# Performance work log

Measured on AMD Instinct MI355X. Metric: run time of the kernel, lower is better.

Reference implementation:

```python
import jax, jax.numpy as jnp
import numpy as np

DIM = 512
N = 64
DIV = 8
H = DIM // DIV  # 64
BATCH = 8
L_SEQ = 2048


def _kernel_dplr(Lam, P, B, C, step, L):
    # Lam: (N,) complex, P: (N,1), B: (N,H), C: (H,N), step: scalar
    omega = jnp.exp(-2j * jnp.pi * (jnp.arange(L) / L))        # (L,)
    g = (2.0 / step) * (1.0 - omega) / (1.0 + omega)           # (L,) generating-fn nodes
    c = 2.0 / (1.0 + omega)                                    # (L,)
    r = 1.0 / (g[:, None] - Lam[None, :])                      # (L,N) Cauchy resolvent
    Cc = jnp.conj(C)                                           # (H,N)
    p = P[:, 0]                                                # (N,)
    pc = jnp.conj(p)
    # vectorized Cauchy dot-products (torch version loops over L)
    k00 = jnp.einsum('in,nj,ln->lij', Cc, B, r)                # (L,H,H)
    k01 = jnp.einsum('in,n,ln->li', Cc, p, r)                  # (L,H)
    k10 = jnp.einsum('n,nj,ln->lj', pc, B, r)                  # (L,H)
    k11 = jnp.einsum('n,n,ln->l', pc, p, r)                    # (L,)
    # woodbury correction: inv(1 + k11) is a 1x1 batched inverse -> elementwise
    at_roots = c[:, None, None] * (
        k00 - k01[:, :, None] * (1.0 / (1.0 + k11))[:, None, None] * k10[:, None, :]
    )                                                          # (L,H,H)
    return jnp.fft.ifft(at_roots, n=L, axis=0).real            # (L,H,H)


def _fft_conv(u, K):
    # u: (b,L,H) real, K: (L,H,H) real. Linear conv via length-2L FFT.
    L = K.shape[0]
    ud = jnp.fft.rfft(u, n=2 * L, axis=1)                      # (b,Lf,H)
    Kd = jnp.fft.rfft(K, n=2 * L, axis=0)                      # (Lf,H,H)
    yf = jnp.einsum('lij,blj->bli', Kd, ud)                    # (b,Lf,H)
    return jnp.fft.irfft(yf, n=2 * L, axis=1)[:, :L]           # (b,L,H)


def reference(u, Lambda_re, Lambda_im, P_re, P_im, B_re, B_im, C_re, C_im, step):
    # straight-through clamp of Lambda_re (torch does an in-place no_grad clamp)
    Lambda_re = Lambda_re + jax.lax.stop_gradient(
        jnp.minimum(Lambda_re, -1e-4) - Lambda_re)
    Lam = Lambda_re + 1j * Lambda_im                           # (N,div)
    P = P_re + 1j * P_im                                       # (N,1,div)
    Bm = B_re + 1j * B_im                                      # (N,H,div)
    Cm = C_re + 1j * C_im                                      # (H,N,div)
    b, L, d = u.shape
    u4 = u.reshape(b, L, d // DIV, DIV)                        # (b,L,H,div)
    s = jnp.exp(step)[0]
    K = jax.vmap(_kernel_dplr, in_axes=(-1, -1, -1, -1, None, None),
                 out_axes=-1)(Lam, P, Bm, Cm, s, L)            # (L,H,H,div)
    y = jax.vmap(_fft_conv, in_axes=(-1, -1), out_axes=-1)(u4, K)  # (b,L,H,div)
    return y.reshape(b, L, d)


def setup_inputs() -> dict:
    key = jax.random.key(0)
    ks = jax.random.split(key, 10)
    sc = 0.5 ** 0.5
    u = jax.random.normal(ks[0], (BATCH, L_SEQ, DIM), dtype=jnp.float32)
    Lambda_re = -(jax.random.uniform(ks[1], (N, DIV), dtype=jnp.float32) * 0.5 + 0.1)
    Lambda_im = jax.random.normal(ks[2], (N, DIV), dtype=jnp.float32)
    P_re = jax.random.normal(ks[3], (N, 1, DIV), dtype=jnp.float32) * sc
    P_im = jax.random.normal(ks[4], (N, 1, DIV), dtype=jnp.float32) * sc
    B_re = jax.random.normal(ks[5], (N, H, DIV), dtype=jnp.float32) * sc
    B_im = jax.random.normal(ks[6], (N, H, DIV), dtype=jnp.float32) * sc
    C_re = jax.random.normal(ks[7], (H, N, DIV), dtype=jnp.float32) * sc
    C_im = jax.random.normal(ks[8], (H, N, DIV), dtype=jnp.float32) * sc
    step = jax.random.uniform(ks[9], (1,), dtype=jnp.float32,
                              minval=float(np.log(0.001)), maxval=float(np.log(0.1)))
    return {"u": u, "Lambda_re": Lambda_re, "Lambda_im": Lambda_im,
            "P_re": P_re, "P_im": P_im, "B_re": B_re, "B_im": B_im,
            "C_re": C_re, "C_im": C_im, "step": step}
```

## Files before the change

kernel.cpp:

```cpp
#include <hip/hip_runtime.h>
#include <hip/hip_bf16.h>
#include <math.h>

#define LSEQ 2048
#define NM   64
#define HD   64
#define NDIV 8
#define NB   8
#define NF   2049
#define ATROWS 4224

#define SL(E) ((E) + ((E) >> 3))
#define FFT_BUF 2304

typedef __attribute__((ext_vector_type(8))) short bf16x8;
typedef __attribute__((ext_vector_type(4))) float f32x4;

__device__ __forceinline__ unsigned pack_c(float2 v) {
  __hip_bfloat162 h = __float22bfloat162_rn(v);
  return *reinterpret_cast<unsigned*>(&h);
}
__device__ __forceinline__ float2 unpack_c(unsigned u) {
  __hip_bfloat162 h = *reinterpret_cast<__hip_bfloat162*>(&u);
  return __bfloat1622float2(h);
}
__device__ __forceinline__ unsigned short f2bf(float v) {
  __hip_bfloat16 h = __float2bfloat16(v);
  return *reinterpret_cast<unsigned short*>(&h);
}

struct cplxd { double x, y; };
__device__ __forceinline__ cplxd cmuld(cplxd a, cplxd b) {
  return {a.x*b.x - a.y*b.y, a.x*b.y + a.y*b.x};
}
__device__ __forceinline__ cplxd cdivd(cplxd a, cplxd b) {
  double inv = 1.0 / (b.x*b.x + b.y*b.y);
  return {(a.x*b.x + a.y*b.y)*inv, (a.y*b.x - a.x*b.y)*inv};
}

template<int SIGN, int M>
__device__ __forceinline__ void r4_stage(const float2* __restrict__ src,
                                         float2* __restrict__ dst) {
  constexpr int L = 2048 / (4 * M);
  __syncthreads();
  #pragma unroll
  for (int t = 0; t < 2; t++) {
    int idx = (int)threadIdx.x + t * 256;
    int q = idx / M;
    int p = idx & (M - 1);
    float2 a0 = src[SL(idx)];
    float2 a1 = src[SL(idx + 512)];
    float2 a2 = src[SL(idx + 1024)];
    float2 a3 = src[SL(idx + 1536)];
    float2 b1, b2, b3;
    if constexpr (M > 1) {
      float s, c;
      __sincosf(-3.14159265358979324f * (float)(p * L) * (1.0f/1024.0f), &s, &c);
      float2 W1 = make_float2(c, (SIGN > 0) ? -s : s);
      float2 W2 = make_float2(W1.x*W1.x - W1.y*W1.y, 2.f*W1.x*W1.y);
      float2 W3 = make_float2(W2.x*W1.x - W2.y*W1.y, W2.x*W1.y + W2.y*W1.x);
      b1 = make_float2(a1.x*W1.x - a1.y*W1.y, a1.x*W1.y + a1.y*W1.x);
      b2 = make_float2(a2.x*W2.x - a2.y*W2.y, a2.x*W2.y + a2.y*W2.x);
      b3 = make_float2(a3.x*W3.x - a3.y*W3.y, a3.x*W3.y + a3.y*W3.x);
    } else { b1 = a1; b2 = a2; b3 = a3; }
    float2 e0 = make_float2(a0.x + b2.x, a0.y + b2.y);
    float2 e1 = make_float2(b1.x + b3.x, b1.y + b3.y);
    float2 d0 = make_float2(a0.x - b2.x, a0.y - b2.y);
    float2 d1 = make_float2(b1.x - b3.x, b1.y - b3.y);
    float2 o1, o3;
    if (SIGN < 0) { o1 = make_float2(d0.x + d1.y, d0.y - d1.x);
                    o3 = make_float2(d0.x - d1.y, d0.y + d1.x); }
    else          { o1 = make_float2(d0.x - d1.y, d0.y + d1.x);
                    o3 = make_float2(d0.x + d1.y, d0.y - d1.x); }
    int ob = q * 4 * M + p;
    dst[SL(ob)]         = make_float2(e0.x + e1.x, e0.y + e1.y);
    dst[SL(ob + M)]     = o1;
    dst[SL(ob + 2*M)]   = make_float2(e0.x - e1.x, e0.y - e1.y);
    dst[SL(ob + 3*M)]   = o3;
  }
}

template<int SIGN>
__device__ __forceinline__ void r4_mid(float2* a, float2* b) {
  r4_stage<SIGN,   4>(a, b);
  r4_stage<SIGN,  16>(b, a);
  r4_stage<SIGN,  64>(a, b);
  r4_stage<SIGN, 256>(b, a);
}

template<int SIGN>
__device__ __forceinline__ void r2f_ldst(const float2* __restrict__ src,
                                         float2* __restrict__ dst) {
  __syncthreads();
  #pragma unroll
  for (int t = 0; t < 4; t++) {
    int p = (int)threadIdx.x + t * 256;
    float2 a = src[SL(p)], b = src[SL(p + 1024)];
    float s, c;
    __sincosf(-6.28318530717958647f * (float)p * (1.0f/2048.0f), &s, &c);
    float wy = (SIGN > 0) ? -s : s;
    float2 wb = make_float2(b.x*c - b.y*wy, b.x*wy + b.y*c);
    dst[SL(p)]        = make_float2(a.x + wb.x, a.y + wb.y);
    dst[SL(p + 1024)] = make_float2(a.x - wb.x, a.y - wb.y);
  }
}

__device__ __forceinline__ void r4g_bf16_inv(const unsigned* __restrict__ row,
                                             float2* __restrict__ dst) {
  #pragma unroll
  for (int t = 0; t < 2; t++) {
    int idx = (int)threadIdx.x + t * 256;
    float2 a0 = unpack_c(row[idx]);
    float2 a1 = unpack_c(row[idx + 512]);
    float2 a2 = unpack_c(row[idx + 1024]);
    float2 a3 = unpack_c(row[idx + 1536]);
    float2 e0 = make_float2(a0.x + a2.x, a0.y + a2.y);
    float2 e1 = make_float2(a1.x + a3.x, a1.y + a3.y);
    float2 d0 = make_float2(a0.x - a2.x, a0.y - a2.y);
    float2 d1 = make_float2(a1.x - a3.x, a1.y - a3.y);
    float2 o1 = make_float2(d0.x - d1.y, d0.y + d1.x);
    float2 o3 = make_float2(d0.x + d1.y, d0.y - d1.x);
    int ob = idx * 4;
    dst[SL(ob)]   = make_float2(e0.x + e1.x, e0.y + e1.y);
    dst[SL(ob+1)] = o1;
    dst[SL(ob+2)] = make_float2(e0.x - e1.x, e0.y - e1.y);
    dst[SL(ob+3)] = o3;
  }
}

__device__ __forceinline__ void r4g_f32pad_fwd(const float2* __restrict__ g,
                                               float2* __restrict__ dst) {
  #pragma unroll
  for (int t = 0; t < 2; t++) {
    int idx = (int)threadIdx.x + t * 256;
    float2 a0 = g[idx];
    float2 a1 = g[idx + 512];
    int ob = idx * 4;
    dst[SL(ob)]   = make_float2(a0.x + a1.x, a0.y + a1.y);
    dst[SL(ob+1)] = make_float2(a0.x + a1.y, a0.y - a1.x);
    dst[SL(ob+2)] = make_float2(a0.x - a1.x, a0.y - a1.y);
    dst[SL(ob+3)] = make_float2(a0.x - a1.y, a0.y + a1.x);
  }
}

__device__ __forceinline__ void r4_modfused(const float2* __restrict__ pre,
                                            float2* __restrict__ dst) {
  __syncthreads();
  const float sc = 1.0f/2048.0f;
  const float R = 0.70710678118654752f;
  #pragma unroll
  for (int t = 0; t < 2; t++) {
    int idx = (int)threadIdx.x + t * 256;
    float a0x = pre[SL(idx)].x;
    float a1x = pre[SL(idx + 512)].x;
    float2 bA = pre[SL(idx + 1024)];
    float2 bB = pre[SL(idx + 1536)];
    float sA, cA, sB, cB;
    __sincosf(-6.28318530717958647f * (float)idx * (1.0f/2048.0f), &sA, &cA);
    __sincosf(-6.28318530717958647f * (float)(idx + 512) * (1.0f/2048.0f), &sB, &cB);
    float rA = bA.x*cA + bA.y*sA;
    float rB = bB.x*cB + bB.y*sB;
    float k0 = (a0x + rA) * sc;
    float k1 = (a1x + rB) * sc;
    float k2 = (a0x - rA) * sc;
    float k3 = (a1x - rB) * sc;
    float s, c;
    __sincosf(-3.14159265358979324f * (float)idx * (1.0f/2048.0f), &s, &c);
    float2 a0 = make_float2(k0*c,         k0*s);
    float2 a1 = make_float2(k1*R*(c + s), k1*R*(s - c));
    float2 a2 = make_float2(k2*s,        -k2*c);
    float2 a3 = make_float2(k3*R*(s - c), -k3*R*(s + c));
    float2 e0 = make_float2(a0.x + a2.x, a0.y + a2.y);
    float2 e1 = make_float2(a1.x + a3.x, a1.y + a3.y);
    float2 d0 = make_float2(a0.x - a2.x, a0.y - a2.y);
    float2 d1 = make_float2(a1.x - a3.x, a1.y - a3.y);
    float2 o1 = make_float2(d0.x + d1.y, d0.y - d1.x);
    float2 o3 = make_float2(d0.x - d1.y, d0.y + d1.x);
    int ob = idx * 4;
    dst[SL(ob)]   = make_float2(e0.x + e1.x, e0.y + e1.y);
    dst[SL(ob+1)] = o1;
    dst[SL(ob+2)] = make_float2(e0.x - e1.x, e0.y - e1.y);
    dst[SL(ob+3)] = o3;
  }
}

__device__ __forceinline__ void r2f_gw_bf16(const float2* __restrict__ src,
                                            unsigned* __restrict__ row) {
  __syncthreads();
  #pragma unroll
  for (int t = 0; t < 4; t++) {
    int p = (int)threadIdx.x + t * 256;
    float2 a = src[SL(p)], b = src[SL(p + 1024)];
    float s, c;
    __sincosf(-6.28318530717958647f * (float)p * (1.0f/2048.0f), &s, &c);
    float2 wb = make_float2(b.x*c - b.y*s, b.x*s + b.y*c);
    row[2*p + 1] = pack_c(make_float2(a.x + wb.x, a.y + wb.y));
  }
}

__device__ __forceinline__ void r2f_gw_f32h(const float2* __restrict__ src,
                                            float2* __restrict__ dst) {
  __syncthreads();
  const float sc = 1.0f/2048.0f;
  #pragma unroll
  for (int t = 0; t < 4; t++) {
    int p = (int)threadIdx.x + t * 256;
    float2 a = src[SL(p)], b = src[SL(p + 1024)];
    float s, c;
    __sincosf(-6.28318530717958647f * (float)p * (1.0f/2048.0f), &s, &c);
    float wy = -s;
    float2 wb = make_float2(b.x*c - b.y*wy, b.x*wy + b.y*c);
    dst[p] = make_float2((a.x + wb.x)*sc, (a.y + wb.y)*sc);
  }
}

__global__ __launch_bounds__(256) void ssm_kt(
    const float* __restrict__ Cre, const float* __restrict__ Cim,
    const float* __restrict__ Bre, const float* __restrict__ Bim,
    const float* __restrict__ Pre, const float* __restrict__ Pim,
    float2* __restrict__ CT, float2* __restrict__ BT, float2* __restrict__ PT) {
  int idx = blockIdx.x * 256 + threadIdx.x;
  int dv = idx >> 12, n = (idx >> 6) & 63, x = idx & 63;
  CT[idx] = make_float2(Cre[((size_t)x*NM + n)*NDIV + dv], -Cim[((size_t)x*NM + n)*NDIV + dv]);
  BT[idx] = make_float2(Bre[((size_t)n*HD + x)*NDIV + dv],  Bim[((size_t)n*HD + x)*NDIV + dv]);
  if (idx < NDIV*NM) {
    int dv2 = idx >> 6, n2 = idx & 63;
    PT[idx] = make_float2(Pre[n2*NDIV + dv2], Pim[n2*NDIV + dv2]);
  }
}

__global__ __launch_bounds__(256) void ssm_k0a(
    const float* __restrict__ Lre, const float* __restrict__ Lim,
    const float* __restrict__ Pre, const float* __restrict__ Pim,
    const float* __restrict__ step, unsigned short* __restrict__ RBr,
    unsigned short* __restrict__ RBi, float2* __restrict__ cpx) {
  int idx = blockIdx.x * 256 + threadIdx.x;
  int qn = idx & 3;
  int rest = idx >> 2;
  int l = rest & (LSEQ - 1);
  int dv = rest >> 11;
  double s = (double)expf(step[0]);
  float angf = -6.2831855f * ((float)l * (1.0f/2048.0f));
  double si, co;
  sincos((double)angf, &si, &co);
  cplxd om    = {co, si};
  cplxd one_p = {1.0 + om.x,  om.y};
  double ts = 2.0 / s;
  cplxd g = cdivd({ts*(1.0 - om.x), ts*(-om.y)}, one_p);
  cplxd c = cdivd({2.0, 0.0}, one_p);
  double k11x = 0.0, k11y = 0.0;
  for (int u = 0; u < 16; u++) {
    int n = qn*16 + u;
    float lre = fminf(Lre[n*NDIV+dv], -0.0001f);
    float lim = Lim[n*NDIV+dv];
    cplxd den = {g.x - (double)lre, g.y - (double)lim};
    cplxd r   = cdivd({1.0, 0.0}, den);
    cplxd rcv = cmuld(c, r);
    size_t bidx = (((size_t)(dv*8 + (n >> 3)))*LSEQ + l)*8 + (n & 7);
    RBr[bidx] = f2bf((float)rcv.x);
    RBi[bidx] = f2bf((float)rcv.y);
    double pr = (double)Pre[n*NDIV+dv], pi = (double)Pim[n*NDIV+dv];
    double p2 = pr*pr + pi*pi;
    k11x += p2 * rcv.x; k11y += p2 * rcv.y;
  }
  k11x += __shfl_xor(k11x, 1); k11y += __shfl_xor(k11y, 1);
  k11x += __shfl_xor(k11x, 2); k11y += __shfl_xor(k11y, 2);
  if (qn == 0)
    cpx[(size_t)dv*LSEQ + l] = make_float2((float)(c.x + k11x), (float)(c.y + k11y));
}

__global__ __launch_bounds__(256) void ssm_km(
    const float2* __restrict__ CT, const float2* __restrict__ BT,
    const float2* __restrict__ PT, unsigned short* __restrict__ ATr,
    unsigned short* __restrict__ ATi, unsigned short* __restrict__ ATin) {
  __shared__ float2 PAN[4096];
  __shared__ float2 ROW[64];
  int dv = blockIdx.y;
  int ib = blockIdx.x;
  int tid = threadIdx.x;
  if (ib < 64) {
    for (int q = tid; q < 4096; q += 256) PAN[q] = BT[(size_t)dv*4096 + q];
    if (tid < 64) ROW[tid] = CT[(size_t)dv*4096 + tid*64 + ib];
    __syncthreads();
    int j = tid >> 2, nq = tid & 3;
    size_t rbase = ((size_t)dv*ATROWS + ib*64 + j)*64;
    for (int u = 0; u < 16; u++) {
      int n = nq*16 + u;
      float2 cv = ROW[n];
      float2 bv = PAN[n*64 + j];
      float xr = cv.x*bv.x - cv.y*bv.y, xi = cv.x*bv.y + cv.y*bv.x;
      ATr[rbase + n] = f2bf(xr); ATi[rbase + n] = f2bf(xi); ATin[rbase + n] = f2bf(-xi);
    }
  } else {
    for (int q = tid; q < 4096; q += 256) PAN[q] = CT[(size_t)dv*4096 + q];
    if (tid < 64) ROW[tid] = PT[dv*64 + tid];
    __syncthreads();
    int x = tid >> 2, nq = tid & 3;
    size_t pbase = ((size_t)dv*ATROWS + 4096 + x)*64;
    for (int u = 0; u < 16; u++) {
      int n = nq*16 + u;
      float2 cv = PAN[n*64 + x];
      float2 pv = ROW[n];
      float xr = cv.x*pv.x - cv.y*pv.y, xi = cv.x*pv.y + cv.y*pv.x;
      ATr[pbase + n] = f2bf(xr); ATi[pbase + n] = f2bf(xi); ATin[pbase + n] = f2bf(-xi);
    }
    __syncthreads();
    for (int q = tid; q < 4096; q += 256) PAN[q] = BT[(size_t)dv*4096 + q];
    __syncthreads();
    size_t qbase = ((size_t)dv*ATROWS + 4160 + x)*64;
    for (int u = 0; u < 16; u++) {
      int n = nq*16 + u;
      float2 bv = PAN[n*64 + x];
      float2 pv = ROW[n];
      float xr = pv.x*bv.x + pv.y*bv.y, xi = pv.x*bv.y - pv.y*bv.x;
      ATr[qbase + n] = f2bf(xr); ATi[qbase + n] = f2bf(xi); ATin[qbase + n] = f2bf(-xi);
    }
  }
}

__device__ __forceinline__ void gemm_core(
    const unsigned short* __restrict__ ATr, const unsigned short* __restrict__ ATi,
    const unsigned short* __restrict__ ATin, const unsigned short* __restrict__ RBr,
    const unsigned short* __restrict__ RBi, int dv, int mrow0, int l0, int lane,
    f32x4 accR[4], f32x4 accI[4]) {
  int mloc = lane & 15, kgrp = lane >> 4;
  #pragma unroll
  for (int t = 0; t < 4; t++) {
    accR[t] = (f32x4){0.f, 0.f, 0.f, 0.f};
    accI[t] = (f32x4){0.f, 0.f, 0.f, 0.f};
  }
  size_t abase = ((size_t)dv*ATROWS + mrow0 + mloc)*64 + kgrp*8;
  #pragma unroll
  for (int s = 0; s < 2; s++) {
    bf16x8 ar = *reinterpret_cast<const bf16x8*>(ATr  + abase + s*32);
    bf16x8 ai = *reinterpret_cast<const bf16x8*>(ATi  + abase + s*32);
    bf16x8 an = *reinterpret_cast<const bf16x8*>(ATin + abase + s*32);
    size_t bbase = (((size_t)(dv*8 + s*4 + kgrp))*LSEQ + l0 + mloc)*8;
    #pragma unroll
    for (int t = 0; t < 4; t++) {
      bf16x8 br = *reinterpret_cast<const bf16x8*>(RBr + bbase + t*128);
      bf16x8 bi = *reinterpret_cast<const bf16x8*>(RBi + bbase + t*128);
      accR[t] = __builtin_amdgcn_mfma_f32_16x16x32_bf16(ar, br, accR[t], 0, 0, 0);
      accR[t] = __builtin_amdgcn_mfma_f32_16x16x32_bf16(an, bi, accR[t], 0, 0, 0);
      accI[t] = __builtin_amdgcn_mfma_f32_16x16x32_bf16(ar, bi, accI[t], 0, 0, 0);
      accI[t] = __builtin_amdgcn_mfma_f32_16x16x32_bf16(ai, br, accI[t], 0, 0, 0);
    }
  }
}

__global__ __launch_bounds__(256) void ssm_g1(
    const unsigned short* __restrict__ ATr, const unsigned short* __restrict__ ATi,
    const unsigned short* __restrict__ ATin, const unsigned short* __restrict__ RBr,
    const unsigned short* __restrict__ RBi, const float2* __restrict__ cpx,
    float2* __restrict__ A1h, float2* __restrict__ K10h) {
  int which = blockIdx.x;
  int nBlk = blockIdx.y;
  int dv = blockIdx.z;
  int wave = threadIdx.x >> 6, lane = threadIdx.x & 63;
  int mrow0 = 4096 + which*64 + wave*16;
  int l0 = nBlk * 64;
  f32x4 accR[4], accI[4];
  gemm_core(ATr, ATi, ATin, RBr, RBi, dv, mrow0, l0, lane, accR, accI);
  int rbase = (lane >> 4) * 4;
  #pragma unroll
  for (int t = 0; t < 4; t++) {
    int l = l0 + t*16 + (lane & 15);
    if (which == 0) {
      float2 w = cpx[((size_t)dv << 11) + l];
      float inv = 1.0f / (w.x*w.x + w.y*w.y);
      #pragma unroll
      for (int r = 0; r < 4; r++) {
        int x = wave*16 + rbase + r;
        float sx = accR[t][r], sy = accI[t][r];
        A1h[((size_t)(dv*64 + x))*LSEQ + l] =
            make_float2((sx*w.x + sy*w.y)*inv, (sy*w.x - sx*w.y)*inv);
      }
    } else {
      #pragma unroll
      for (int r = 0; r < 4; r++) {
        int x = wave*16 + rbase + r;
        K10h[((size_t)(dv*LSEQ + l))*64 + x] = make_float2(accR[t][r], accI[t][r]);
      }
    }
  }
}

__global__ __launch_bounds__(256) void ssm_g2(
    const unsigned short* __restrict__ ATr, const unsigned short* __restrict__ ATi,
    const unsigned short* __restrict__ ATin, const unsigned short* __restrict__ RBr,
    const unsigned short* __restrict__ RBi, const float2* __restrict__ A1h,
    const float2* __restrict__ K10h, unsigned* __restrict__ big, int dv) {
  int mBlk = blockIdx.x;
  int nBlk = blockIdx.y;
  int wave = threadIdx.x >> 6, lane = threadIdx.x & 63;
  int mrow0 = mBlk*64 + wave*16;
  int l0 = nBlk * 64;
  f32x4 accR[4], accI[4];
  gemm_core(ATr, ATi, ATin, RBr, RBi, dv, mrow0, l0, lane, accR, accI);
  int rbase = (lane >> 4) * 4;
  #pragma unroll
  for (int t = 0; t < 4; t++) {
    int l = l0 + t*16 + (lane & 15);
    float2 a1 = A1h[((size_t)(dv*64 + mBlk))*LSEQ + l];
    const float2* kp = K10h + ((size_t)(dv*LSEQ + l))*64 + wave*16 + rbase;
    #pragma unroll
    for (int r = 0; r < 4; r++) {
      float2 k10 = kp[r];
      float cx = a1.x*k10.x - a1.y*k10.y;
      float cy = a1.x*k10.y + a1.y*k10.x;
      int chain = mBlk*64 + wave*16 + rbase + r;
      big[(size_t)chain*NF + l] = pack_c(make_float2(accR[t][r] - cx, accI[t][r] - cy));
    }
  }
}

__global__ __launch_bounds__(256) void ssm_ku(const float* __restrict__ u, float* __restrict__ ut) {
  __shared__ float s[16][513];
  int b  = blockIdx.x >> 7;
  int l0 = (blockIdx.x & 127) << 4;
  int tid = threadIdx.x;
  for (int q = tid; q < 16*512; q += 256) {
    int ll = q >> 9, dd = q & 511;
    s[ll][dd] = u[((size_t)b*LSEQ + l0 + ll)*512 + dd];
  }
  __syncthreads();
  for (int q = tid; q < 16*512; q += 256) {
    int d = q >> 4, ll = q & 15;
    int dvv = d & 7, h = d >> 3;
    ut[(((size_t)(dvv*NB + b))*HD + h)*LSEQ + l0 + ll] = s[ll][d];
  }
}

__global__ __launch_bounds__(256) void ssm_k3(const float* __restrict__ ut,
                                              float2* __restrict__ ud, int cbase) {
  __shared__ float2 b0[FFT_BUF];
  __shared__ float2 b1[FFT_BUF];
  int tid = threadIdx.x;
  const float2* src = (const float2*)(ut + ((size_t)(cbase + blockIdx.x)) * LSEQ);
  float2* dst = ud + (size_t)blockIdx.x * NF;
  r4g_f32pad_fwd(src, b1);
  r4_mid<-1>(b1, b0);
  r2f_ldst<-1>(b1, b0);
  __syncthreads();
  for (int f = tid; f <= 2048; f += 256) {
    int fa = f & 2047, fb = (2048 - f) & 2047;
    float2 Zf = b0[SL(fa)];
    float2 Zm = b0[SL(fb)];
    float Ex = (Zf.x + Zm.x)*0.5f, Ey = (Zf.y - Zm.y)*0.5f;
    float Dx = Zf.x - Zm.x,        Dy = Zf.y + Zm.y;
    float Ox = Dy*0.5f, Oy = -Dx*0.5f;
    float s, c2;
    __sincosf(-6.28318530717958647f * (float)f * (1.0f/4096.0f), &s, &c2);
    float WOx = Ox*c2 - Oy*s, WOy = Ox*s + Oy*c2;
    dst[f] = make_float2(Ex + WOx, Ey + WOy);
  }
}

__global__ __launch_bounds__(256) void ssm_k2(unsigned* __restrict__ big) {
  __shared__ float2 b0[FFT_BUF];
  __shared__ float2 b1[FFT_BUF];
  int tid = threadIdx.x;
  unsigned* row = big + (size_t)blockIdx.x * NF;
  float2 ev[4];
  #pragma unroll
  for (int k = 0; k < 4; k++) {
    int l = tid + 256*k;
    float2 a = unpack_c(row[l]);
    float2 b = unpack_c(row[(2048 - l) & 2047]);
    ev[k] = make_float2((a.x + b.x)*0.5f, (a.y - b.y)*0.5f);
  }
  float ev1024 = (tid == 0) ? unpack_c(row[1024]).x : 0.f;
  r4g_bf16_inv(row, b1);
  __syncthreads();
  #pragma unroll
  for (int k = 0; k < 4; k++) { int l = tid + 256*k; row[2*l] = pack_c(ev[k]); }
  if (tid == 0) row[2048] = pack_c(make_float2(ev1024, 0.f));
  r4_mid<1>(b1, b0);
  r4_modfused(b1, b0);
  r4_mid<-1>(b0, b1);
  r2f_gw_bf16(b0, row);
}

__global__ __launch_bounds__(256) void ssm_k4(
    const unsigned* __restrict__ kdt, const float2* __restrict__ ud,
    float2* __restrict__ yf) {
  __shared__ float2 uds[NB][32][16];
  int tid = threadIdx.x;
  int f0 = blockIdx.x * 16;
  int i0 = blockIdx.y * 16;
  int ii = tid >> 4, ff = tid & 15;
  int i = i0 + ii;
  int f = f0 + ff;
  int fr = (f < NF) ? f : 2048;
  float2 acc[NB];
  #pragma unroll
  for (int b = 0; b < NB; b++) acc[b] = make_float2(0.f, 0.f);
  for (int jh = 0; jh < 2; jh++) {
    __syncthreads();
    for (int q = tid; q < NB*32*16; q += 256) {
      int b = q >> 9, j = (q >> 4) & 31, fq = q & 15;
      int f_ = f0 + fq;
      uds[b][j][fq] = (f_ < NF) ? ud[((size_t)(b*HD + jh*32 + j))*NF + f_]
                                : make_float2(0.f, 0.f);
    }
    __syncthreads();
    for (int j = 0; j < 32; j++) {
      float2 kv = unpack_c(kdt[((size_t)(i*HD + jh*32 + j))*NF + fr]);
      #pragma unroll
      for (int b = 0; b < NB; b++) {
        float2 uv = uds[b][j][ff];
        acc[b].x += kv.x*uv.x - kv.y*uv.y;
        acc[b].y += kv.x*uv.y + kv.y*uv.x;
      }
    }
  }
  if (f < NF) {
    #pragma unroll
    for (int b = 0; b < NB; b++)
      yf[((size_t)(b*HD + i))*NF + f] = acc[b];
  }
}

__global__ __launch_bounds__(256) void ssm_k5(const float2* __restrict__ yf,
                                              float* __restrict__ yt, int dv) {
  __shared__ float2 b0[FFT_BUF];
  __shared__ float2 b1[FFT_BUF];
  int tid = threadIdx.x;
  int b = blockIdx.x >> 6, i = blockIdx.x & 63;
  const float2* src = yf + (size_t)(b*HD + i) * NF;
  float2* dst = (float2*)(yt + (((size_t)(dv*NB + b))*HD + i) * LSEQ);
  for (int k = tid; k < 2048; k += 256) {
    float2 Xk = src[k];
    float2 Xm = src[2048 - k];
    float Ex = (Xk.x + Xm.x)*0.5f, Ey = (Xk.y - Xm.y)*0.5f;
    float Dx = Xk.x - Xm.x,        Dy = Xk.y + Xm.y;
    float s, c;
    __sincosf(6.28318530717958647f * (float)k * (1.0f/4096.0f), &s, &c);
    float Ox = 0.5f*(Dx*c - Dy*s);
    float Oy = 0.5f*(Dx*s + Dy*c);
    b0[SL(k)] = make_float2(Ex - Oy, Ey + Ox);
  }
  r4_stage<1, 1>(b0, b1);
  r4_mid<1>(b1, b0);
  r2f_gw_f32h(b1, dst);
}

__global__ __launch_bounds__(256) void ssm_t2(const float* __restrict__ yt, float* __restrict__ out) {
  __shared__ float s[512][17];
  int b  = blockIdx.x >> 7;
  int t0 = (blockIdx.x & 127) << 4;
  int tid = threadIdx.x;
  for (int q = tid; q < 512*16; q += 256) {
    int d = q >> 4, tt = q & 15;
    int dvv = d & 7, i = d >> 3;
    s[d][tt] = yt[(((size_t)(dvv*NB + b))*HD + i)*LSEQ + t0 + tt];
  }
  __syncthreads();
  for (int q = tid; q < 512*16; q += 256) {
    int tt = q >> 9, d = q & 511;
    out[((size_t)b*LSEQ + t0 + tt)*512 + d] = s[d][tt];
  }
}

extern "C" void kernel_launch(void* const* d_in, const int* in_sizes, int n_in,
                              void* d_out, int out_size, void* d_ws, size_t ws_size,
                              hipStream_t stream) {
  const float* u    = (const float*)d_in[0];
  const float* Lre  = (const float*)d_in[1];
  const float* Lim  = (const float*)d_in[2];
  const float* Pre  = (const float*)d_in[3];
  const float* Pim  = (const float*)d_in[4];
  const float* Bre  = (const float*)d_in[5];
  const float* Bim  = (const float*)d_in[6];
  const float* Cre  = (const float*)d_in[7];
  const float* Cim  = (const float*)d_in[8];
  const float* step = (const float*)d_in[9];
  float* out = (float*)d_out;

  char* w = (char*)d_ws;
  size_t off = 0;
  auto carve = [&](size_t bytes) -> void* {
    void* p = (void*)(w + off);
    off += (bytes + 255) & ~(size_t)255;
    return p;
  };
  float2*   cpx  = (float2*)carve((size_t)NDIV*LSEQ*sizeof(float2));
  float*    ut   = (float*) carve((size_t)NDIV*NB*HD*LSEQ*sizeof(float));
  unsigned* big  = (unsigned*)carve((size_t)4096*NF*sizeof(unsigned));
  float2*   yf   = (float2*)carve((size_t)512*NF*sizeof(float2));
  float2*   CT   = (float2*)carve((size_t)NDIV*NM*HD*sizeof(float2));
  float2*   BT   = (float2*)carve((size_t)NDIV*NM*HD*sizeof(float2));
  float2*   PT   = (float2*)carve((size_t)NDIV*NM*sizeof(float2));
  unsigned short* ATr  = (unsigned short*)carve((size_t)NDIV*ATROWS*64*2);
  unsigned short* ATi  = (unsigned short*)carve((size_t)NDIV*ATROWS*64*2);
  unsigned short* ATin = (unsigned short*)carve((size_t)NDIV*ATROWS*64*2);
  unsigned short* RBr  = (unsigned short*)carve((size_t)NDIV*8*LSEQ*8*2);
  unsigned short* RBi  = (unsigned short*)carve((size_t)NDIV*8*LSEQ*8*2);
  float2*   A1h  = (float2*)carve((size_t)NDIV*64*LSEQ*sizeof(float2));
  float2*   K10h = (float2*)carve((size_t)NDIV*LSEQ*64*sizeof(float2));
  size_t off_m = off;
  float2* ud_full = (float2*)carve((size_t)NDIV*512*NF*sizeof(float2));
  bool full = (ws_size >= off);
  float2* ud = ud_full;
  if (!full) {
    off = off_m;
    ud = (float2*)carve((size_t)512*NF*sizeof(float2));
    if (ws_size < off) return;
  }
  (void)in_sizes; (void)n_in; (void)out_size;

  ssm_kt<<<128, 256, 0, stream>>>(Cre, Cim, Bre, Bim, Pre, Pim, CT, BT, PT);
  ssm_k0a<<<256, 256, 0, stream>>>(Lre, Lim, Pre, Pim, step, RBr, RBi, cpx);
  ssm_km<<<dim3(65, 8), 256, 0, stream>>>(CT, BT, PT, ATr, ATi, ATin);
  ssm_ku<<<1024, 256, 0, stream>>>(u, ut);
  ssm_g1<<<dim3(2, 32, 8), 256, 0, stream>>>(ATr, ATi, ATin, RBr, RBi, cpx, A1h, K10h);
  if (full) ssm_k3<<<4096, 256, 0, stream>>>(ut, ud_full, 0);
  for (int dv = 0; dv < NDIV; ++dv) {
    if (!full) ssm_k3<<<512, 256, 0, stream>>>(ut, ud, dv*512);
    const float2* udp = full ? (ud_full + (size_t)dv*512*NF) : ud;
    ssm_g2<<<dim3(64, 32), 256, 0, stream>>>(ATr, ATi, ATin, RBr, RBi, A1h, K10h, big, dv);
    ssm_k2<<<4096, 256, 0, stream>>>(big);
    ssm_k4<<<dim3(129, 4), 256, 0, stream>>>(big, udp, yf);
    ssm_k5<<<512, 256, 0, stream>>>(yf, ut, dv);
  }
  ssm_t2<<<1024, 256, 0, stream>>>(ut, out);
}
```

Baseline: 951.6 us.

## Register-tile k4 frequency loop, pad kernel rows, store input spectra in bf16

The per-frequency kernel-by-input multiply now processes four frequencies per thread from 128-bit vector loads of a kernel spectrum whose rows are padded to a multiple of four (NFP). The block frequency tile grows from 16 to 64, so far fewer blocks are launched and each kernel load is reused across more accumulators. The input spectra written by k3 are packed to bf16 complex, halving their storage and the bandwidth k4 spends reading them, at the cost of precision. Register pressure rises with 32 complex accumulators per thread. Reads in the last tile go past frequency 2048 into the padding; those values are loaded but never stored.

```diff
diff --git a/kernel.cpp b/kernel.cpp
--- a/kernel.cpp
+++ b/kernel.cpp
@@ -8,6 +8,7 @@
 #define NDIV 8
 #define NB   8
 #define NF   2049
+#define NFP  2052
 #define ATROWS 4224
 
 #define SL(E) ((E) + ((E) >> 3))
@@ -409,7 +410,7 @@
       float cx = a1.x*k10.x - a1.y*k10.y;
       float cy = a1.x*k10.y + a1.y*k10.x;
       int chain = mBlk*64 + wave*16 + rbase + r;
-      big[(size_t)chain*NF + l] = pack_c(make_float2(accR[t][r] - cx, accI[t][r] - cy));
+      big[(size_t)chain*NFP + l] = pack_c(make_float2(accR[t][r] - cx, accI[t][r] - cy));
     }
   }
 }
@@ -432,12 +433,12 @@
 }
 
 __global__ __launch_bounds__(256) void ssm_k3(const float* __restrict__ ut,
-                                              float2* __restrict__ ud, int cbase) {
+                                              unsigned* __restrict__ ud, int cbase) {
   __shared__ float2 b0[FFT_BUF];
   __shared__ float2 b1[FFT_BUF];
   int tid = threadIdx.x;
   const float2* src = (const float2*)(ut + ((size_t)(cbase + blockIdx.x)) * LSEQ);
-  float2* dst = ud + (size_t)blockIdx.x * NF;
+  unsigned* dst = ud + (size_t)blockIdx.x * NF;
   r4g_f32pad_fwd(src, b1);
   r4_mid<-1>(b1, b0);
   r2f_ldst<-1>(b1, b0);
@@ -452,7 +453,7 @@
     float s, c2;
     __sincosf(-6.28318530717958647f * (float)f * (1.0f/4096.0f), &s, &c2);
     float WOx = Ox*c2 - Oy*s, WOy = Ox*s + Oy*c2;
-    dst[f] = make_float2(Ex + WOx, Ey + WOy);
+    dst[f] = pack_c(make_float2(Ex + WOx, Ey + WOy));
   }
 }
 
@@ -460,7 +461,7 @@
   __shared__ float2 b0[FFT_BUF];
   __shared__ float2 b1[FFT_BUF];
   int tid = threadIdx.x;
-  unsigned* row = big + (size_t)blockIdx.x * NF;
+  unsigned* row = big + (size_t)blockIdx.x * NFP;
   float2 ev[4];
   #pragma unroll
   for (int k = 0; k < 4; k++) {
@@ -482,42 +483,50 @@
 }
 
 __global__ __launch_bounds__(256) void ssm_k4(
-    const unsigned* __restrict__ kdt, const float2* __restrict__ ud,
+    const unsigned* __restrict__ kdt, const unsigned* __restrict__ ud,
     float2* __restrict__ yf) {
-  __shared__ float2 uds[NB][32][16];
+  __shared__ float2 uds[NB][8][64];
   int tid = threadIdx.x;
-  int f0 = blockIdx.x * 16;
+  int f0 = blockIdx.x * 64;
   int i0 = blockIdx.y * 16;
-  int ii = tid >> 4, ff = tid & 15;
+  int ii = tid >> 4, fq4 = tid & 15;
   int i = i0 + ii;
-  int f = f0 + ff;
-  int fr = (f < NF) ? f : 2048;
-  float2 acc[NB];
-  #pragma unroll
-  for (int b = 0; b < NB; b++) acc[b] = make_float2(0.f, 0.f);
-  for (int jh = 0; jh < 2; jh++) {
+  float2 acc[4][NB];
+  #pragma unroll
+  for (int e = 0; e < 4; e++)
+    #pragma unroll
+    for (int b = 0; b < NB; b++) acc[e][b] = make_float2(0.f, 0.f);
+  for (int jc = 0; jc < 8; jc++) {
     __syncthreads();
-    for (int q = tid; q < NB*32*16; q += 256) {
-      int b = q >> 9, j = (q >> 4) & 31, fq = q & 15;
+    for (int q = tid; q < NB*8*64; q += 256) {
+      int b = q >> 9, j = (q >> 6) & 7, fq = q & 63;
       int f_ = f0 + fq;
-      uds[b][j][fq] = (f_ < NF) ? ud[((size_t)(b*HD + jh*32 + j))*NF + f_]
+      uds[b][j][fq] = (f_ < NF) ? unpack_c(ud[((size_t)(b*HD + jc*8 + j))*NF + f_])
                                 : make_float2(0.f, 0.f);
     }
     __syncthreads();
-    for (int j = 0; j < 32; j++) {
-      float2 kv = unpack_c(kdt[((size_t)(i*HD + jh*32 + j))*NF + fr]);
+    #pragma unroll 2
+    for (int j = 0; j < 8; j++) {
+      const unsigned* kp = kdt + ((size_t)(i*HD + jc*8 + j))*NFP + f0 + fq4*4;
+      uint4 kq = *reinterpret_cast<const uint4*>(kp);
+      float2 kv[4] = {unpack_c(kq.x), unpack_c(kq.y), unpack_c(kq.z), unpack_c(kq.w)};
       #pragma unroll
       for (int b = 0; b < NB; b++) {
-        float2 uv = uds[b][j][ff];
-        acc[b].x += kv.x*uv.x - kv.y*uv.y;
-        acc[b].y += kv.x*uv.y + kv.y*uv.x;
+        #pragma unroll
+        for (int e = 0; e < 4; e++) {
+          float2 uv = uds[b][j][fq4*4 + e];
+          acc[e][b].x += kv[e].x*uv.x - kv[e].y*uv.y;
+          acc[e][b].y += kv[e].x*uv.y + kv[e].y*uv.x;
+        }
       }
     }
   }
-  if (f < NF) {
+  #pragma unroll
+  for (int b = 0; b < NB; b++) {
+    size_t base = ((size_t)(b*HD + i))*NF + f0 + fq4*4;
     #pragma unroll
-    for (int b = 0; b < NB; b++)
-      yf[((size_t)(b*HD + i))*NF + f] = acc[b];
+    for (int e = 0; e < 4; e++)
+      if (f0 + fq4*4 + e < NF) yf[base + e] = acc[e][b];
   }
 }
 
@@ -586,7 +595,7 @@
   };
   float2*   cpx  = (float2*)carve((size_t)NDIV*LSEQ*sizeof(float2));
   float*    ut   = (float*) carve((size_t)NDIV*NB*HD*LSEQ*sizeof(float));
-  unsigned* big  = (unsigned*)carve((size_t)4096*NF*sizeof(unsigned));
+  unsigned* big  = (unsigned*)carve((size_t)4096*NFP*sizeof(unsigned) + 256);
   float2*   yf   = (float2*)carve((size_t)512*NF*sizeof(float2));
   float2*   CT   = (float2*)carve((size_t)NDIV*NM*HD*sizeof(float2));
   float2*   BT   = (float2*)carve((size_t)NDIV*NM*HD*sizeof(float2));
@@ -599,12 +608,12 @@
   float2*   A1h  = (float2*)carve((size_t)NDIV*64*LSEQ*sizeof(float2));
   float2*   K10h = (float2*)carve((size_t)NDIV*LSEQ*64*sizeof(float2));
   size_t off_m = off;
-  float2* ud_full = (float2*)carve((size_t)NDIV*512*NF*sizeof(float2));
+  unsigned* ud_full = (unsigned*)carve((size_t)NDIV*512*NF*sizeof(unsigned));
   bool full = (ws_size >= off);
-  float2* ud = ud_full;
+  unsigned* ud = ud_full;
   if (!full) {
     off = off_m;
-    ud = (float2*)carve((size_t)512*NF*sizeof(float2));
+    ud = (unsigned*)carve((size_t)512*NF*sizeof(unsigned));
     if (ws_size < off) return;
   }
   (void)in_sizes; (void)n_in; (void)out_size;
@@ -617,10 +626,10 @@
   if (full) ssm_k3<<<4096, 256, 0, stream>>>(ut, ud_full, 0);
   for (int dv = 0; dv < NDIV; ++dv) {
     if (!full) ssm_k3<<<512, 256, 0, stream>>>(ut, ud, dv*512);
-    const float2* udp = full ? (ud_full + (size_t)dv*512*NF) : ud;
+    const unsigned* udp = full ? (ud_full + (size_t)dv*512*NF) : ud;
     ssm_g2<<<dim3(64, 32), 256, 0, stream>>>(ATr, ATi, ATin, RBr, RBi, A1h, K10h, big, dv);
     ssm_k2<<<4096, 256, 0, stream>>>(big);
-    ssm_k4<<<dim3(129, 4), 256, 0, stream>>>(big, udp, yf);
+    ssm_k4<<<dim3(33, 4), 256, 0, stream>>>(big, udp, yf);
     ssm_k5<<<512, 256, 0, stream>>>(yf, ut, dv);
   }
   ssm_t2<<<1024, 256, 0, stream>>>(ut, out);
```

Result: slower. 1.585 ms (+66.5%).
